# Kernel optimization log

Measured on AMD Instinct MI355X. Metric: run time of the kernel, lower is better.

Reference implementation:

```python
import jax, jax.numpy as jnp
import numpy as np

B, T, I, H, O = 128, 256, 64, 1024, 64


def setup_inputs() -> dict:
    key = jax.random.key(0)
    ks = jax.random.split(key, 16)
    s_ih1 = 1.0 / np.sqrt(H)
    def mk(k, shape, s):
        return jax.random.uniform(k, shape, jnp.float32, -s, s)
    return {
        "x": jax.random.normal(ks[0], (B, T, I), jnp.float32),
        # RNNCell 1: input I -> hidden H
        "W_ih1": mk(ks[1], (H, I), s_ih1),
        "b_ih1": mk(ks[2], (H,), s_ih1),
        "W_hh1": mk(ks[3], (H, H), s_ih1),
        "b_hh1": mk(ks[4], (H,), s_ih1),
        # RNNCell 2: hidden H -> hidden H
        "W_ih2": mk(ks[5], (H, H), s_ih1),
        "b_ih2": mk(ks[6], (H,), s_ih1),
        "W_hh2": mk(ks[7], (H, H), s_ih1),
        "b_hh2": mk(ks[8], (H,), s_ih1),
        # gate: 2H -> H
        "Wg": mk(ks[9], (H, 2 * H), 1.0 / np.sqrt(2 * H)),
        "bg": mk(ks[10], (H,), 1.0 / np.sqrt(2 * H)),
        # output heads: H -> O
        "Wo1": mk(ks[11], (O, H), s_ih1),
        "bo1": mk(ks[12], (O,), s_ih1),
        "Wo2": mk(ks[13], (O, H), s_ih1),
        "bo2": mk(ks[14], (O,), s_ih1),
    }


def reference(x, W_ih1, b_ih1, W_hh1, b_hh1, W_ih2, b_ih2, W_hh2, b_hh2,
              Wg, bg, Wo1, bo1, Wo2, bo2):
    batch = x.shape[0]
    h1_0 = jnp.zeros((batch, H), x.dtype)
    h2_0 = jnp.zeros((batch, H), x.dtype)
    u_0 = jnp.ones((batch, H), x.dtype)

    def step(carry, x_t):
        h1, h2, u = carry
        # RNNCell 1
        h1 = jnp.tanh(x_t @ W_ih1.T + b_ih1 + h1 @ W_hh1.T + b_hh1)
        # RNNCell 2, gated convex blend with previous h2
        h2_new = jnp.tanh(h1 @ W_ih2.T + b_ih2 + h2 @ W_hh2.T + b_hh2)
        h2 = u * h2_new + (1.0 - u) * h2
        # dual tanh output head
        out = jnp.tanh(h1 @ Wo1.T + bo1) + jnp.tanh(h2 @ Wo2.T + bo2)
        # gate for NEXT step, computed from current hiddens
        u = jax.nn.sigmoid(jnp.concatenate([h1, h2], axis=1) @ Wg.T + bg)
        return (h1, h2, u), out

    xs = jnp.swapaxes(x, 0, 1)  # [T, B, I]
    _, outs = jax.lax.scan(step, (h1_0, h2_0, u_0), xs)
    return jnp.swapaxes(outs, 0, 1)  # [B, T, O]
```

## Files before the change

kernel.cpp:

```cpp
#include <hip/hip_runtime.h>
#include <cstddef>

using bf16x8 = __attribute__((ext_vector_type(8))) short;
using f32x4  = __attribute__((ext_vector_type(4))) float;

constexpr int Bb = 128;
constexpr int Tt = 256;
constexpr int Hh = 1024;
constexpr int Oo = 64;
constexpr int NBLK = 168;
constexpr int FLAG_STRIDE = 32;
constexpr int RS = 1048;

__device__ __forceinline__ float bf2f(short s) {
  unsigned int u = ((unsigned int)(unsigned short)s) << 16;
  float f;
  __builtin_memcpy(&f, &u, 4);
  return f;
}
__device__ __forceinline__ short f2bf(float f) {
  unsigned int u;
  __builtin_memcpy(&u, &f, 4);
  u += 0x7fffu + ((u >> 16) & 1u);
  return (short)(u >> 16);
}
__device__ __forceinline__ bf16x8 as_bf(int4 v) {
  union { int4 i; bf16x8 b; } u; u.i = v; return u.b;
}
__device__ __forceinline__ float ldf(const float* p) {
  return __hip_atomic_load((float*)p, __ATOMIC_RELAXED, __HIP_MEMORY_SCOPE_AGENT);
}
__device__ __forceinline__ void stf(float* p, float v) {
  __hip_atomic_store(p, v, __ATOMIC_RELAXED, __HIP_MEMORY_SCOPE_AGENT);
}
__device__ __forceinline__ unsigned ldu(const unsigned* p) {
  return __hip_atomic_load((unsigned*)p, __ATOMIC_RELAXED, __HIP_MEMORY_SCOPE_AGENT);
}

#define LD16A(d, p) asm volatile("global_load_dwordx4 %0, %1, off sc1" \
                                 : "=v"(d) : "v"((const void*)(p)))

__device__ __forceinline__ void stage32(short* As, const short* src, int tid) {
  const int row = tid >> 3;
  const int c0  = (tid & 7) * 8;
  const short* gp = src + (size_t)row * Hh + c0;
  short* lp = As + row * RS + c0;
  int4 r0[8], r1[8];
#pragma unroll
  for (int j = 0; j < 8; ++j) LD16A(r0[j], gp + j * 64);
#pragma unroll
  for (int j = 0; j < 8; ++j) LD16A(r1[j], gp + 512 + j * 64);
  asm volatile("s_waitcnt vmcnt(8)" ::: "memory");
#pragma unroll
  for (int j = 0; j < 8; ++j) *(int4*)(lp + j * 64) = r0[j];
  asm volatile("s_waitcnt vmcnt(0)" ::: "memory");
#pragma unroll
  for (int j = 0; j < 8; ++j) *(int4*)(lp + 512 + j * 64) = r1[j];
}

struct BPre {
  const short *bp0, *bp1;
  int4 b0v[6], b1v[6];
};
__device__ __forceinline__ void prefillB(BPre& P,
    const short* __restrict__ B0, size_t st0,
    const short* __restrict__ B1, size_t st1, int lm, int q) {
  P.bp0 = B0 + (size_t)lm * st0 + q * 8;
  P.bp1 = B1 + (size_t)lm * st1 + q * 8;
#pragma unroll
  for (int c = 0; c < 5; ++c) {
    P.b0v[c] = *(const int4*)(P.bp0 + c * 32);
    P.b1v[c] = *(const int4*)(P.bp1 + c * 32);
  }
}
__device__ __forceinline__ void pass32p(const short* As, int lm, int q,
    BPre& P, f32x4 (&acc)[2][2]) {
  const short* ap0 = As + lm * RS + q * 8;
  const short* ap1 = ap0 + 16 * RS;
#pragma unroll
  for (int c = 0; c < 32; ++c) {
    if (c + 5 < 32) {
      P.b0v[(c + 5) % 6] = *(const int4*)(P.bp0 + (c + 5) * 32);
      P.b1v[(c + 5) % 6] = *(const int4*)(P.bp1 + (c + 5) * 32);
    }
    const bf16x8 a0 = as_bf(*(const int4*)(ap0 + c * 32));
    const bf16x8 a1 = as_bf(*(const int4*)(ap1 + c * 32));
    const bf16x8 b0 = as_bf(P.b0v[c % 6]);
    const bf16x8 b1 = as_bf(P.b1v[c % 6]);
    acc[0][0] = __builtin_amdgcn_mfma_f32_16x16x32_bf16(a0, b0, acc[0][0], 0, 0, 0);
    acc[0][1] = __builtin_amdgcn_mfma_f32_16x16x32_bf16(a1, b0, acc[0][1], 0, 0, 0);
    acc[1][0] = __builtin_amdgcn_mfma_f32_16x16x32_bf16(a0, b1, acc[1][0], 0, 0, 0);
    acc[1][1] = __builtin_amdgcn_mfma_f32_16x16x32_bf16(a1, b1, acc[1][1], 0, 0, 0);
  }
}

__device__ __forceinline__ void grid_barrier(unsigned* flags,
                                             unsigned gen, int bid, int tid) {
  __builtin_amdgcn_s_waitcnt(0);
  __syncthreads();
  if (tid == 0)
    __hip_atomic_store(flags + (size_t)bid * FLAG_STRIDE, gen,
                       __ATOMIC_RELAXED, __HIP_MEMORY_SCOPE_AGENT);
  if (tid < 64) {
    const unsigned* f = flags + (size_t)tid * FLAG_STRIDE;
    for (;;) {
      const unsigned a = ldu(f);
      const unsigned b = ldu(f +  64 * FLAG_STRIDE);
      const unsigned c = ldu(f + 128 * FLAG_STRIDE);
      if (__all((a >= gen) && (b >= gen) && (c >= gen))) break;
      __builtin_amdgcn_s_sleep(1);
    }
  }
  __syncthreads();
  asm volatile("" ::: "memory");
}

#define ST_BF16_PAIR(BASE, ROW, COL, HV) do {                              \
    const int _ov = __shfl_xor((int)(unsigned short)(HV), 1, 64);          \
    if ((lm & 1) == 0) {                                                   \
      const unsigned _pk = (unsigned)(unsigned short)(HV) | ((unsigned)_ov << 16); \
      __hip_atomic_store((unsigned*)((BASE) + (size_t)(ROW) * Hh + (COL)), _pk, \
                         __ATOMIC_RELAXED, __HIP_MEMORY_SCOPE_AGENT);      \
    } } while (0)

struct RP {
  short *h1a, *h1b;
  short *h2a, *h2b;
  float *h2f;
  float *pre2f;
  float *pg1f;
  float *po1f;
  const short* prex;
  const short *whh1, *wih2, *whh2, *wg, *wo1, *wo2;
  const float *b_ih2, *b_hh2, *bg, *bo1, *bo2;
  float* out;
  unsigned *flags;
};

__global__ void __launch_bounds__(256, 1) rnn_kernel(RP p) {
  __shared__ short As[32 * RS];
  const int tid = threadIdx.x;
  const int lane = tid & 63;
  const int wv = tid >> 6;
  const int lm = lane & 15;
  const int q = lane >> 4;
  const int bid = blockIdx.x;

  int role, mb, cb;
  if      (bid < 32)  { role = 0; mb = (bid >> 3) * 32;         cb = (bid & 7) * 128; }
  else if (bid < 64)  { role = 1; mb = ((bid - 32) >> 3) * 32;  cb = ((bid - 32) & 7) * 128; }
  else if (bid < 96)  { role = 2; mb = ((bid - 64) >> 3) * 32;  cb = ((bid - 64) & 7) * 128; }
  else if (bid < 100) { role = 3; mb = (bid - 96) * 32;         cb = 0; }
  else if (bid < 164) { role = 4; mb = ((bid - 100) >> 4) * 32; cb = ((bid - 100) & 15) * 64; }
  else                { role = 5; mb = (bid - 164) * 32;        cb = 0; }

  int colw;
  if (role == 4) colw = cb + wv * 16;
  else if (role == 3 || role == 5) colw = (wv & 1) * 32;
  else colw = cb + wv * 32;

  float bias0 = 0.f, bias1 = 0.f;
  if (role == 1) {
    bias0 = p.b_ih2[colw + lm] + p.b_hh2[colw + lm];
    bias1 = p.b_ih2[colw + 16 + lm] + p.b_hh2[colw + 16 + lm];
  } else if (role == 2) {
    bias0 = p.bg[colw + lm]; bias1 = p.bg[colw + 16 + lm];
  } else if (role == 3) {
    bias0 = p.bo1[colw + lm]; bias1 = p.bo1[colw + 16 + lm];
  } else if (role == 5) {
    bias0 = p.bo2[colw + lm]; bias1 = p.bo2[colw + 16 + lm];
  }

  const short* B0; const short* B1;
  size_t st0 = Hh, st1 = Hh;
  if      (role == 0) { B0 = p.whh1 + (size_t)colw * Hh; B1 = p.whh1 + (size_t)(colw + 16) * Hh; }
  else if (role == 1) { B0 = p.wih2 + (size_t)colw * Hh; B1 = p.wih2 + (size_t)(colw + 16) * Hh; }
  else if (role == 2) { B0 = p.wg + (size_t)colw * (2 * Hh); B1 = p.wg + (size_t)(colw + 16) * (2 * Hh); st0 = st1 = 2 * Hh; }
  else if (role == 3) { B0 = p.wo1 + (size_t)colw * Hh; B1 = p.wo1 + (size_t)(colw + 16) * Hh; }
  else if (role == 4) { B0 = p.whh2 + (size_t)colw * Hh; B1 = p.wg + Hh + (size_t)colw * (2 * Hh); st1 = 2 * Hh; }
  else                { B0 = p.wo2 + (size_t)colw * Hh; B1 = p.wo2 + (size_t)(colw + 16) * Hh; }

  const size_t HS = (size_t)Bb * Hh;
  const f32x4 z4 = {0.f, 0.f, 0.f, 0.f};
  unsigned gen = 0;

  for (int ph = 0; ph <= Tt + 2; ++ph) {
    const short* h1prev = (ph & 1) ? p.h1a : p.h1b;
    short*       h1out  = (ph & 1) ? p.h1b : p.h1a;
    const int s = ph - 2;
    const short* h2prev = (s & 1) ? p.h2a : p.h2b;
    short*       h2out  = (s & 1) ? p.h2b : p.h2a;

    if (role == 0) {
      if (ph < Tt) {
        BPre P; prefillB(P, B0, st0, B1, st1, lm, q);
        short prs[2][2][4];
        const short* pr = p.prex + (size_t)ph * HS;
#pragma unroll
        for (int n = 0; n < 2; ++n)
#pragma unroll
          for (int rf = 0; rf < 2; ++rf)
#pragma unroll
            for (int r = 0; r < 4; ++r)
              prs[n][rf][r] = pr[(size_t)(mb + rf * 16 + q * 4 + r) * Hh + colw + n * 16 + lm];
        stage32(As, h1prev + (size_t)mb * Hh, tid);
        __syncthreads();
        f32x4 acc[2][2]; acc[0][0] = acc[0][1] = acc[1][0] = acc[1][1] = z4;
        pass32p(As, lm, q, P, acc);
#pragma unroll
        for (int n = 0; n < 2; ++n)
#pragma unroll
          for (int rf = 0; rf < 2; ++rf)
#pragma unroll
            for (int r = 0; r < 4; ++r) {
              const int row = mb + rf * 16 + q * 4 + r;
              const int col = colw + n * 16 + lm;
              const short hv = f2bf(tanhf(acc[n][rf][r] + bf2f(prs[n][rf][r])));
              ST_BF16_PAIR(h1out, row, col, hv);
            }
      }
    } else if (role == 1) {
      if (ph >= 1 && ph <= Tt) {
        BPre P; prefillB(P, B0, st0, B1, st1, lm, q);
        float* dst = p.pre2f + (size_t)((ph - 1) & 1) * HS;
        stage32(As, h1prev + (size_t)mb * Hh, tid);
        __syncthreads();
        f32x4 acc[2][2]; acc[0][0] = acc[0][1] = acc[1][0] = acc[1][1] = z4;
        pass32p(As, lm, q, P, acc);
#pragma unroll
        for (int n = 0; n < 2; ++n)
#pragma unroll
          for (int rf = 0; rf < 2; ++rf)
#pragma unroll
            for (int r = 0; r < 4; ++r) {
              const int row = mb + rf * 16 + q * 4 + r;
              const int col = colw + n * 16 + lm;
              stf(dst + (size_t)row * Hh + col, acc[n][rf][r] + (n ? bias1 : bias0));
            }
      }
    } else if (role == 2) {
      if (ph >= 1 && ph <= Tt) {
        BPre P; prefillB(P, B0, st0, B1, st1, lm, q);
        float* dst = p.pg1f + (size_t)((ph - 1) % 3) * HS;
        stage32(As, h1prev + (size_t)mb * Hh, tid);
        __syncthreads();
        f32x4 acc[2][2]; acc[0][0] = acc[0][1] = acc[1][0] = acc[1][1] = z4;
        pass32p(As, lm, q, P, acc);
#pragma unroll
        for (int n = 0; n < 2; ++n)
#pragma unroll
          for (int rf = 0; rf < 2; ++rf)
#pragma unroll
            for (int r = 0; r < 4; ++r) {
              const int row = mb + rf * 16 + q * 4 + r;
              const int col = colw + n * 16 + lm;
              stf(dst + (size_t)row * Hh + col, acc[n][rf][r] + (n ? bias1 : bias0));
            }
      }
    } else if (role == 3) {
      if (ph >= 1 && ph <= Tt) {
        BPre P;
        if (wv < 2) prefillB(P, B0, st0, B1, st1, lm, q);
        float* dst = p.po1f + (size_t)((ph - 1) % 3) * (Bb * Oo);
        stage32(As, h1prev + (size_t)mb * Hh, tid);
        __syncthreads();
        if (wv < 2) {
          f32x4 acc[2][2]; acc[0][0] = acc[0][1] = acc[1][0] = acc[1][1] = z4;
          pass32p(As, lm, q, P, acc);
#pragma unroll
          for (int n = 0; n < 2; ++n)
#pragma unroll
            for (int rf = 0; rf < 2; ++rf)
#pragma unroll
              for (int r = 0; r < 4; ++r) {
                const int row = mb + rf * 16 + q * 4 + r;
                const int col = colw + n * 16 + lm;
                stf(dst + (size_t)row * Oo + col,
                    tanhf(acc[n][rf][r] + (n ? bias1 : bias0)));
              }
        }
      }
    } else if (role == 4) {
      if (ph >= 2 && ph <= Tt + 1) {
        BPre P; prefillB(P, B0, st0, B1, st1, lm, q);
        float p2v[2][4], pg1v[2][4], hpv[2][4];
        const float* pre2s = p.pre2f + (size_t)(s & 1) * HS;
        const float* pg1s  = p.pg1f + (size_t)((s + 2) % 3) * HS;
#pragma unroll
        for (int rf = 0; rf < 2; ++rf)
#pragma unroll
          for (int r = 0; r < 4; ++r) {
            const size_t idx = (size_t)(mb + rf * 16 + q * 4 + r) * Hh + colw + lm;
            p2v[rf][r] = ldf(pre2s + idx);
            pg1v[rf][r] = (s > 0) ? ldf(pg1s + idx) : 0.f;
            hpv[rf][r] = p.h2f[idx];
          }
        stage32(As, h2prev + (size_t)mb * Hh, tid);
        __syncthreads();
        f32x4 acc[2][2]; acc[0][0] = acc[0][1] = acc[1][0] = acc[1][1] = z4;
        pass32p(As, lm, q, P, acc);
#pragma unroll
        for (int rf = 0; rf < 2; ++rf)
#pragma unroll
          for (int r = 0; r < 4; ++r) {
            const int row = mb + rf * 16 + q * 4 + r;
            const int col = colw + lm;
            const size_t idx = (size_t)row * Hh + col;
            const float u = (s == 0) ? 1.f
                : 1.f / (1.f + expf(-(acc[1][rf][r] + pg1v[rf][r])));
            const float hn = tanhf(acc[0][rf][r] + p2v[rf][r]);
            const float nv = fmaf(u, hn - hpv[rf][r], hpv[rf][r]);
            p.h2f[idx] = nv;
            const short hv = f2bf(nv);
            ST_BF16_PAIR(h2out, row, col, hv);
          }
      }
    } else {
      if (ph >= 3) {
        const int to = ph - 3;
        BPre P;
        if (wv < 2) prefillB(P, B0, st0, B1, st1, lm, q);
        const float* po1s = p.po1f + (size_t)(to % 3) * (Bb * Oo);
        float pv[2][2][4];
        if (wv < 2) {
#pragma unroll
          for (int n = 0; n < 2; ++n)
#pragma unroll
            for (int rf = 0; rf < 2; ++rf)
#pragma unroll
              for (int r = 0; r < 4; ++r)
                pv[n][rf][r] = ldf(po1s + (size_t)(mb + rf * 16 + q * 4 + r) * Oo
                                   + colw + n * 16 + lm);
        }
        stage32(As, h2prev + (size_t)mb * Hh, tid);
        __syncthreads();
        if (wv < 2) {
          f32x4 acc[2][2]; acc[0][0] = acc[0][1] = acc[1][0] = acc[1][1] = z4;
          pass32p(As, lm, q, P, acc);
#pragma unroll
          for (int n = 0; n < 2; ++n)
#pragma unroll
            for (int rf = 0; rf < 2; ++rf)
#pragma unroll
              for (int r = 0; r < 4; ++r) {
                const int row = mb + rf * 16 + q * 4 + r;
                const int col = colw + n * 16 + lm;
                p.out[(size_t)row * (Tt * Oo) + (size_t)to * Oo + col] =
                    pv[n][rf][r] + tanhf(acc[n][rf][r] + (n ? bias1 : bias0));
              }
        }
      }
    }
    ++gen;
    grid_barrier(p.flags, gen, bid, tid);
  }
}

__global__ void __launch_bounds__(256) prex_kernel(
    const float* __restrict__ x, const float* __restrict__ wih1,
    const float* __restrict__ b_ih1, const float* __restrict__ b_hh1,
    short* __restrict__ prex) {
  const int tid = threadIdx.x;
  const int lane = tid & 63;
  const int wv = tid >> 6;
  const int lm = lane & 15;
  const int q = lane >> 4;
  const int bm = blockIdx.x >> 4;
  const int bn = blockIdx.x & 15;
  const int rowbase = bm * 64;
  const int col = bn * 64 + wv * 16 + lm;

  const f32x4 z4 = {0.f, 0.f, 0.f, 0.f};
  f32x4 acc[4];
#pragma unroll
  for (int mt = 0; mt < 4; ++mt) acc[mt] = z4;

#pragma unroll
  for (int kc = 0; kc < 2; ++kc) {
    const float* bp = wih1 + col * 64 + kc * 32 + q * 8;
    bf16x8 bf;
#pragma unroll
    for (int j = 0; j < 8; ++j) bf[j] = f2bf(bp[j]);
#pragma unroll
    for (int mt = 0; mt < 4; ++mt) {
      const float* ap = x + (size_t)(rowbase + mt * 16 + lm) * 64 + kc * 32 + q * 8;
      bf16x8 af;
#pragma unroll
      for (int j = 0; j < 8; ++j) af[j] = f2bf(ap[j]);
      acc[mt] = __builtin_amdgcn_mfma_f32_16x16x32_bf16(af, bf, acc[mt], 0, 0, 0);
    }
  }
  const float bia = b_ih1[col] + b_hh1[col];
#pragma unroll
  for (int mt = 0; mt < 4; ++mt) {
#pragma unroll
    for (int r = 0; r < 4; ++r) {
      const int row = rowbase + mt * 16 + q * 4 + r;
      const int b  = row >> 8;
      const int tt = row & 255;
      prex[((size_t)tt * Bb + b) * Hh + col] = f2bf(acc[mt][r] + bia);
    }
  }
}

__global__ void conv_kernel(const float* __restrict__ s, short* __restrict__ d, int n) {
  int i = blockIdx.x * blockDim.x + threadIdx.x;
  const int stride = gridDim.x * blockDim.x;
  for (; i < n; i += stride) d[i] = f2bf(s[i]);
}

__global__ void init_kernel(short* h1a, short* h1b, short* h2a, short* h2b,
                            float* h2f, unsigned* flags) {
  const int i = blockIdx.x * blockDim.x + threadIdx.x;
  h1a[i] = 0; h1b[i] = 0; h2a[i] = 0; h2b[i] = 0; h2f[i] = 0.f;
  if (i < 256) flags[i * FLAG_STRIDE] = (i < NBLK) ? 0u : 0xFFFFFFFFu;
}

extern "C" void kernel_launch(void* const* d_in, const int* in_sizes, int n_in,
                              void* d_out, int out_size, void* d_ws, size_t ws_size,
                              hipStream_t stream) {
  (void)in_sizes; (void)n_in; (void)out_size; (void)ws_size;
  const float* x      = (const float*)d_in[0];
  const float* W_ih1  = (const float*)d_in[1];
  const float* b_ih1  = (const float*)d_in[2];
  const float* W_hh1  = (const float*)d_in[3];
  const float* b_hh1  = (const float*)d_in[4];
  const float* W_ih2  = (const float*)d_in[5];
  const float* b_ih2  = (const float*)d_in[6];
  const float* W_hh2  = (const float*)d_in[7];
  const float* b_hh2  = (const float*)d_in[8];
  const float* Wg     = (const float*)d_in[9];
  const float* bg     = (const float*)d_in[10];
  const float* Wo1    = (const float*)d_in[11];
  const float* bo1    = (const float*)d_in[12];
  const float* Wo2    = (const float*)d_in[13];
  const float* bo2    = (const float*)d_in[14];

  char* ws = (char*)d_ws;
  size_t off = 0;
  auto alloc = [&](size_t bytes) -> void* {
    void* ptr = ws + off;
    off += (bytes + 255) & ~(size_t)255;
    return ptr;
  };
  short* whh1 = (short*)alloc((size_t)Hh * Hh * 2);
  short* wih2 = (short*)alloc((size_t)Hh * Hh * 2);
  short* whh2 = (short*)alloc((size_t)Hh * Hh * 2);
  short* wg   = (short*)alloc((size_t)Hh * 2 * Hh * 2);
  short* wo1  = (short*)alloc((size_t)Oo * Hh * 2);
  short* wo2  = (short*)alloc((size_t)Oo * Hh * 2);
  short* prex = (short*)alloc((size_t)Bb * Tt * Hh * 2);
  short* h1a  = (short*)alloc((size_t)Bb * Hh * 2);
  short* h1b  = (short*)alloc((size_t)Bb * Hh * 2);
  short* h2a  = (short*)alloc((size_t)Bb * Hh * 2);
  short* h2b  = (short*)alloc((size_t)Bb * Hh * 2);
  float* h2f  = (float*)alloc((size_t)Bb * Hh * 4);
  float* pre2f= (float*)alloc((size_t)2 * Bb * Hh * 4);
  float* pg1f = (float*)alloc((size_t)3 * Bb * Hh * 4);
  float* po1f = (float*)alloc((size_t)3 * Bb * Oo * 4);
  unsigned* flags = (unsigned*)alloc(256 * FLAG_STRIDE * 4);

  conv_kernel<<<1024, 256, 0, stream>>>(W_hh1, whh1, Hh * Hh);
  conv_kernel<<<1024, 256, 0, stream>>>(W_ih2, wih2, Hh * Hh);
  conv_kernel<<<1024, 256, 0, stream>>>(W_hh2, whh2, Hh * Hh);
  conv_kernel<<<2048, 256, 0, stream>>>(Wg,    wg,   Hh * 2 * Hh);
  conv_kernel<<<256,  256, 0, stream>>>(Wo1,   wo1,  Oo * Hh);
  conv_kernel<<<256,  256, 0, stream>>>(Wo2,   wo2,  Oo * Hh);
  init_kernel<<<512, 256, 0, stream>>>(h1a, h1b, h2a, h2b, h2f, flags);
  prex_kernel<<<8192, 256, 0, stream>>>(x, W_ih1, b_ih1, b_hh1, prex);

  RP p;
  p.h1a = h1a; p.h1b = h1b; p.h2a = h2a; p.h2b = h2b;
  p.h2f = h2f; p.pre2f = pre2f; p.pg1f = pg1f; p.po1f = po1f;
  p.prex = prex;
  p.whh1 = whh1; p.wih2 = wih2; p.whh2 = whh2;
  p.wg = wg; p.wo1 = wo1; p.wo2 = wo2;
  p.b_ih2 = b_ih2; p.b_hh2 = b_hh2;
  p.bg = bg; p.bo1 = bo1; p.bo2 = bo2;
  p.out = (float*)d_out;
  p.flags = flags;

  rnn_kernel<<<NBLK, 256, 0, stream>>>(p);
}
```

Measured before the change: 3.234 ms.

## Replace global grid barrier with per-role dataflow flags and triple-buffered state

Removes the all-block grid barrier after each phase and replaces it with per-producer generation flags, so each role polls only the producer groups it depends on. Hidden-state buffers become triple-buffered and the intermediate buffers get three or four slots, which lets roles run a few steps apart without overwriting data still being read. This aims to cut barrier latency and let the h1 chain run ahead of the h2 chain. The cost is more complex dependency tracking, where a wrong slot count or wait condition could cause races.

```diff
diff --git a/kernel.cpp b/kernel.cpp
--- a/kernel.cpp
+++ b/kernel.cpp
@@ -12,6 +12,13 @@
 constexpr int FLAG_STRIDE = 32;
 constexpr int RS = 1048;
 
+constexpr int FH1 = 0;
+constexpr int FP2 = 32;
+constexpr int FPG = 64;
+constexpr int FPO = 96;
+constexpr int FH2 = 100;
+constexpr int FZO = 164;
+
 __device__ __forceinline__ float bf2f(short s) {
   unsigned int u = ((unsigned int)(unsigned short)s) << 16;
   float f;
@@ -35,6 +42,13 @@
 }
 __device__ __forceinline__ unsigned ldu(const unsigned* p) {
   return __hip_atomic_load((unsigned*)p, __ATOMIC_RELAXED, __HIP_MEMORY_SCOPE_AGENT);
+}
+__device__ __forceinline__ short* sel3(short* a, short* b, short* c, int i) {
+  return i == 0 ? a : (i == 1 ? b : c);
+}
+__device__ __forceinline__ const short* sel3c(const short* a, const short* b,
+                                              const short* c, int i) {
+  return i == 0 ? a : (i == 1 ? b : c);
 }
 
 #define LD16A(d, p) asm volatile("global_load_dwordx4 %0, %1, off sc1" \
@@ -94,26 +108,20 @@
   }
 }
 
-__device__ __forceinline__ void grid_barrier(unsigned* flags,
-                                             unsigned gen, int bid, int tid) {
-  __builtin_amdgcn_s_waitcnt(0);
-  __syncthreads();
-  if (tid == 0)
-    __hip_atomic_store(flags + (size_t)bid * FLAG_STRIDE, gen,
-                       __ATOMIC_RELAXED, __HIP_MEMORY_SCOPE_AGENT);
-  if (tid < 64) {
-    const unsigned* f = flags + (size_t)tid * FLAG_STRIDE;
-    for (;;) {
-      const unsigned a = ldu(f);
-      const unsigned b = ldu(f +  64 * FLAG_STRIDE);
-      const unsigned c = ldu(f + 128 * FLAG_STRIDE);
-      if (__all((a >= gen) && (b >= gen) && (c >= gen))) break;
-      __builtin_amdgcn_s_sleep(1);
-    }
-  }
-  __syncthreads();
-  asm volatile("" ::: "memory");
-}
+__device__ __forceinline__ void poll_ge(const unsigned* flags, int base,
+                                        int mask, unsigned gen) {
+  const unsigned* f = flags + (size_t)(base + (threadIdx.x & mask)) * FLAG_STRIDE;
+  while (!__all(ldu(f) >= gen))
+    __builtin_amdgcn_s_sleep(2);
+}
+
+#define POST_FLAG(GEN) do {                                                \
+    asm volatile("s_waitcnt vmcnt(0) lgkmcnt(0)" ::: "memory");            \
+    __syncthreads();                                                       \
+    if (tid == 0)                                                          \
+      __hip_atomic_store(p.flags + (size_t)bid * FLAG_STRIDE, (unsigned)(GEN), \
+                         __ATOMIC_RELAXED, __HIP_MEMORY_SCOPE_AGENT);      \
+  } while (0)
 
 #define ST_BF16_PAIR(BASE, ROW, COL, HV) do {                              \
     const int _ov = __shfl_xor((int)(unsigned short)(HV), 1, 64);          \
@@ -124,8 +132,8 @@
     } } while (0)
 
 struct RP {
-  short *h1a, *h1b;
-  short *h2a, *h2b;
+  short *h1r0, *h1r1, *h1r2;
+  short *h2r0, *h2r1, *h2r2;
   float *h2f;
   float *pre2f;
   float *pg1f;
@@ -134,7 +142,7 @@
   const short *whh1, *wih2, *whh2, *wg, *wo1, *wo2;
   const float *b_ih2, *b_hh2, *bg, *bo1, *bo2;
   float* out;
-  unsigned *flags;
+  unsigned* flags;
 };
 
 __global__ void __launch_bounds__(256, 1) rnn_kernel(RP p) {
@@ -182,31 +190,115 @@
 
   const size_t HS = (size_t)Bb * Hh;
   const f32x4 z4 = {0.f, 0.f, 0.f, 0.f};
-  unsigned gen = 0;
-
-  for (int ph = 0; ph <= Tt + 2; ++ph) {
-    const short* h1prev = (ph & 1) ? p.h1a : p.h1b;
-    short*       h1out  = (ph & 1) ? p.h1b : p.h1a;
-    const int s = ph - 2;
-    const short* h2prev = (s & 1) ? p.h2a : p.h2b;
-    short*       h2out  = (s & 1) ? p.h2b : p.h2a;
-
-    if (role == 0) {
-      if (ph < Tt) {
-        BPre P; prefillB(P, B0, st0, B1, st1, lm, q);
-        short prs[2][2][4];
-        const short* pr = p.prex + (size_t)ph * HS;
-#pragma unroll
-        for (int n = 0; n < 2; ++n)
-#pragma unroll
-          for (int rf = 0; rf < 2; ++rf)
-#pragma unroll
-            for (int r = 0; r < 4; ++r)
-              prs[n][rf][r] = pr[(size_t)(mb + rf * 16 + q * 4 + r) * Hh + colw + n * 16 + lm];
-        stage32(As, h1prev + (size_t)mb * Hh, tid);
-        __syncthreads();
+
+  if (role == 0) {
+    for (int t = 0; t < Tt; ++t) {
+      BPre P; prefillB(P, B0, st0, B1, st1, lm, q);
+      short prs[2][2][4];
+      const short* pr = p.prex + (size_t)t * HS;
+#pragma unroll
+      for (int n = 0; n < 2; ++n)
+#pragma unroll
+        for (int rf = 0; rf < 2; ++rf)
+#pragma unroll
+          for (int r = 0; r < 4; ++r)
+            prs[n][rf][r] = pr[(size_t)(mb + rf * 16 + q * 4 + r) * Hh + colw + n * 16 + lm];
+      if (tid < 64) {
+        if (t >= 1) poll_ge(p.flags, FH1, 31, (unsigned)t);
+        if (t >= 3) {
+          poll_ge(p.flags, FP2, 31, (unsigned)(t - 2));
+          poll_ge(p.flags, FPG, 31, (unsigned)(t - 2));
+          poll_ge(p.flags, FPO, 3,  (unsigned)(t - 2));
+        }
+      }
+      __syncthreads();
+      const short* h1prev = sel3c(p.h1r0, p.h1r1, p.h1r2, (t + 2) % 3);
+      stage32(As, h1prev + (size_t)mb * Hh, tid);
+      __syncthreads();
+      f32x4 acc[2][2]; acc[0][0] = acc[0][1] = acc[1][0] = acc[1][1] = z4;
+      pass32p(As, lm, q, P, acc);
+      short* h1out = sel3(p.h1r0, p.h1r1, p.h1r2, t % 3);
+#pragma unroll
+      for (int n = 0; n < 2; ++n)
+#pragma unroll
+        for (int rf = 0; rf < 2; ++rf)
+#pragma unroll
+          for (int r = 0; r < 4; ++r) {
+            const int row = mb + rf * 16 + q * 4 + r;
+            const int col = colw + n * 16 + lm;
+            const short hv = f2bf(tanhf(acc[n][rf][r] + bf2f(prs[n][rf][r])));
+            ST_BF16_PAIR(h1out, row, col, hv);
+          }
+      POST_FLAG(t + 1);
+    }
+  } else if (role == 1) {
+    for (int t = 0; t < Tt; ++t) {
+      BPre P; prefillB(P, B0, st0, B1, st1, lm, q);
+      if (tid < 64) {
+        poll_ge(p.flags, FH1, 31, (unsigned)(t + 1));
+        if (t >= 3) poll_ge(p.flags, FH2, 63, (unsigned)(t - 2));
+      }
+      __syncthreads();
+      const short* h1cur = sel3c(p.h1r0, p.h1r1, p.h1r2, t % 3);
+      stage32(As, h1cur + (size_t)mb * Hh, tid);
+      __syncthreads();
+      f32x4 acc[2][2]; acc[0][0] = acc[0][1] = acc[1][0] = acc[1][1] = z4;
+      pass32p(As, lm, q, P, acc);
+      float* dst = p.pre2f + (size_t)(t % 3) * HS;
+#pragma unroll
+      for (int n = 0; n < 2; ++n)
+#pragma unroll
+        for (int rf = 0; rf < 2; ++rf)
+#pragma unroll
+          for (int r = 0; r < 4; ++r) {
+            const int row = mb + rf * 16 + q * 4 + r;
+            const int col = colw + n * 16 + lm;
+            stf(dst + (size_t)row * Hh + col, acc[n][rf][r] + (n ? bias1 : bias0));
+          }
+      POST_FLAG(t + 1);
+    }
+  } else if (role == 2) {
+    for (int t = 0; t < Tt; ++t) {
+      BPre P; prefillB(P, B0, st0, B1, st1, lm, q);
+      if (tid < 64) {
+        poll_ge(p.flags, FH1, 31, (unsigned)(t + 1));
+        if (t >= 4) poll_ge(p.flags, FH2, 63, (unsigned)(t - 2));
+      }
+      __syncthreads();
+      const short* h1cur = sel3c(p.h1r0, p.h1r1, p.h1r2, t % 3);
+      stage32(As, h1cur + (size_t)mb * Hh, tid);
+      __syncthreads();
+      f32x4 acc[2][2]; acc[0][0] = acc[0][1] = acc[1][0] = acc[1][1] = z4;
+      pass32p(As, lm, q, P, acc);
+      float* dst = p.pg1f + (size_t)(t % 4) * HS;
+#pragma unroll
+      for (int n = 0; n < 2; ++n)
+#pragma unroll
+        for (int rf = 0; rf < 2; ++rf)
+#pragma unroll
+          for (int r = 0; r < 4; ++r) {
+            const int row = mb + rf * 16 + q * 4 + r;
+            const int col = colw + n * 16 + lm;
+            stf(dst + (size_t)row * Hh + col, acc[n][rf][r] + (n ? bias1 : bias0));
+          }
+      POST_FLAG(t + 1);
+    }
+  } else if (role == 3) {
+    for (int t = 0; t < Tt; ++t) {
+      BPre P;
+      if (wv < 2) prefillB(P, B0, st0, B1, st1, lm, q);
+      if (tid < 64) {
+        poll_ge(p.flags, FH1, 31, (unsigned)(t + 1));
+        if (t >= 4) poll_ge(p.flags, FZO, 3, (unsigned)(t - 3));
+      }
+      __syncthreads();
+      const short* h1cur = sel3c(p.h1r0, p.h1r1, p.h1r2, t % 3);
+      stage32(As, h1cur + (size_t)mb * Hh, tid);
+      __syncthreads();
+      if (wv < 2) {
         f32x4 acc[2][2]; acc[0][0] = acc[0][1] = acc[1][0] = acc[1][1] = z4;
         pass32p(As, lm, q, P, acc);
+        float* dst = p.po1f + (size_t)(t % 4) * (Bb * Oo);
 #pragma unroll
         for (int n = 0; n < 2; ++n)
 #pragma unroll
@@ -215,16 +307,84 @@
             for (int r = 0; r < 4; ++r) {
               const int row = mb + rf * 16 + q * 4 + r;
               const int col = colw + n * 16 + lm;
-              const short hv = f2bf(tanhf(acc[n][rf][r] + bf2f(prs[n][rf][r])));
-              ST_BF16_PAIR(h1out, row, col, hv);
+              stf(dst + (size_t)row * Oo + col,
+                  tanhf(acc[n][rf][r] + (n ? bias1 : bias0)));
             }
       }
-    } else if (role == 1) {
-      if (ph >= 1 && ph <= Tt) {
-        BPre P; prefillB(P, B0, st0, B1, st1, lm, q);
-        float* dst = p.pre2f + (size_t)((ph - 1) & 1) * HS;
-        stage32(As, h1prev + (size_t)mb * Hh, tid);
-        __syncthreads();
+      POST_FLAG(t + 1);
+    }
+  } else if (role == 4) {
+    for (int s = 0; s < Tt; ++s) {
+      BPre P; prefillB(P, B0, st0, B1, st1, lm, q);
+      if (tid < 64) {
+        poll_ge(p.flags, FP2, 31, (unsigned)(s + 1));
+        if (s >= 1) {
+          poll_ge(p.flags, FPG, 31, (unsigned)s);
+          poll_ge(p.flags, FH2, 63, (unsigned)s);
+        }
+        if (s >= 3) poll_ge(p.flags, FZO, 3, (unsigned)(s - 2));
+      }
+      __syncthreads();
+      float p2v[2][4], pg1v[2][4], hpv[2][4];
+      const float* pre2s = p.pre2f + (size_t)(s % 3) * HS;
+      const float* pg1s  = p.pg1f + (size_t)((s + 3) % 4) * HS;
+#pragma unroll
+      for (int rf = 0; rf < 2; ++rf)
+#pragma unroll
+        for (int r = 0; r < 4; ++r) {
+          const size_t idx = (size_t)(mb + rf * 16 + q * 4 + r) * Hh + colw + lm;
+          p2v[rf][r] = ldf(pre2s + idx);
+          pg1v[rf][r] = (s > 0) ? ldf(pg1s + idx) : 0.f;
+          hpv[rf][r] = p.h2f[idx];
+        }
+      const short* h2prev = sel3c(p.h2r0, p.h2r1, p.h2r2, (s + 2) % 3);
+      stage32(As, h2prev + (size_t)mb * Hh, tid);
+      __syncthreads();
+      f32x4 acc[2][2]; acc[0][0] = acc[0][1] = acc[1][0] = acc[1][1] = z4;
+      pass32p(As, lm, q, P, acc);
+      short* h2out = sel3(p.h2r0, p.h2r1, p.h2r2, s % 3);
+#pragma unroll
+      for (int rf = 0; rf < 2; ++rf)
+#pragma unroll
+        for (int r = 0; r < 4; ++r) {
+          const int row = mb + rf * 16 + q * 4 + r;
+          const int col = colw + lm;
+          const size_t idx = (size_t)row * Hh + col;
+          const float u = (s == 0) ? 1.f
+              : 1.f / (1.f + expf(-(acc[1][rf][r] + pg1v[rf][r])));
+          const float hn = tanhf(acc[0][rf][r] + p2v[rf][r]);
+          const float nv = fmaf(u, hn - hpv[rf][r], hpv[rf][r]);
+          p.h2f[idx] = nv;
+          const short hv = f2bf(nv);
+          ST_BF16_PAIR(h2out, row, col, hv);
+        }
+      POST_FLAG(s + 1);
+    }
+  } else {
+    for (int ot = 0; ot < Tt; ++ot) {
+      BPre P;
+      if (wv < 2) prefillB(P, B0, st0, B1, st1, lm, q);
+      if (tid < 64) {
+        poll_ge(p.flags, FH2, 63, (unsigned)(ot + 1));
+        poll_ge(p.flags, FPO, 3,  (unsigned)(ot + 1));
+      }
+      __syncthreads();
+      const float* po1s = p.po1f + (size_t)(ot % 4) * (Bb * Oo);
+      float pv[2][2][4];
+      if (wv < 2) {
+#pragma unroll
+        for (int n = 0; n < 2; ++n)
+#pragma unroll
+          for (int rf = 0; rf < 2; ++rf)
+#pragma unroll
+            for (int r = 0; r < 4; ++r)
+              pv[n][rf][r] = ldf(po1s + (size_t)(mb + rf * 16 + q * 4 + r) * Oo
+                                 + colw + n * 16 + lm);
+      }
+      const short* h2cur = sel3c(p.h2r0, p.h2r1, p.h2r2, ot % 3);
+      stage32(As, h2cur + (size_t)mb * Hh, tid);
+      __syncthreads();
+      if (wv < 2) {
         f32x4 acc[2][2]; acc[0][0] = acc[0][1] = acc[1][0] = acc[1][1] = z4;
         pass32p(As, lm, q, P, acc);
 #pragma unroll
@@ -235,124 +395,12 @@
             for (int r = 0; r < 4; ++r) {
               const int row = mb + rf * 16 + q * 4 + r;
               const int col = colw + n * 16 + lm;
-              stf(dst + (size_t)row * Hh + col, acc[n][rf][r] + (n ? bias1 : bias0));
+              p.out[(size_t)row * (Tt * Oo) + (size_t)ot * Oo + col] =
+                  pv[n][rf][r] + tanhf(acc[n][rf][r] + (n ? bias1 : bias0));
             }
       }
-    } else if (role == 2) {
-      if (ph >= 1 && ph <= Tt) {
-        BPre P; prefillB(P, B0, st0, B1, st1, lm, q);
-        float* dst = p.pg1f + (size_t)((ph - 1) % 3) * HS;
-        stage32(As, h1prev + (size_t)mb * Hh, tid);
-        __syncthreads();
-        f32x4 acc[2][2]; acc[0][0] = acc[0][1] = acc[1][0] = acc[1][1] = z4;
-        pass32p(As, lm, q, P, acc);
-#pragma unroll
-        for (int n = 0; n < 2; ++n)
-#pragma unroll
-          for (int rf = 0; rf < 2; ++rf)
-#pragma unroll
-            for (int r = 0; r < 4; ++r) {
-              const int row = mb + rf * 16 + q * 4 + r;
-              const int col = colw + n * 16 + lm;
-              stf(dst + (size_t)row * Hh + col, acc[n][rf][r] + (n ? bias1 : bias0));
-            }
-      }
-    } else if (role == 3) {
-      if (ph >= 1 && ph <= Tt) {
-        BPre P;
-        if (wv < 2) prefillB(P, B0, st0, B1, st1, lm, q);
-        float* dst = p.po1f + (size_t)((ph - 1) % 3) * (Bb * Oo);
-        stage32(As, h1prev + (size_t)mb * Hh, tid);
-        __syncthreads();
-        if (wv < 2) {
-          f32x4 acc[2][2]; acc[0][0] = acc[0][1] = acc[1][0] = acc[1][1] = z4;
-          pass32p(As, lm, q, P, acc);
-#pragma unroll
-          for (int n = 0; n < 2; ++n)
-#pragma unroll
-            for (int rf = 0; rf < 2; ++rf)
-#pragma unroll
-              for (int r = 0; r < 4; ++r) {
-                const int row = mb + rf * 16 + q * 4 + r;
-                const int col = colw + n * 16 + lm;
-                stf(dst + (size_t)row * Oo + col,
-                    tanhf(acc[n][rf][r] + (n ? bias1 : bias0)));
-              }
-        }
-      }
-    } else if (role == 4) {
-      if (ph >= 2 && ph <= Tt + 1) {
-        BPre P; prefillB(P, B0, st0, B1, st1, lm, q);
-        float p2v[2][4], pg1v[2][4], hpv[2][4];
-        const float* pre2s = p.pre2f + (size_t)(s & 1) * HS;
-        const float* pg1s  = p.pg1f + (size_t)((s + 2) % 3) * HS;
-#pragma unroll
-        for (int rf = 0; rf < 2; ++rf)
-#pragma unroll
-          for (int r = 0; r < 4; ++r) {
-            const size_t idx = (size_t)(mb + rf * 16 + q * 4 + r) * Hh + colw + lm;
-            p2v[rf][r] = ldf(pre2s + idx);
-            pg1v[rf][r] = (s > 0) ? ldf(pg1s + idx) : 0.f;
-            hpv[rf][r] = p.h2f[idx];
-          }
-        stage32(As, h2prev + (size_t)mb * Hh, tid);
-        __syncthreads();
-        f32x4 acc[2][2]; acc[0][0] = acc[0][1] = acc[1][0] = acc[1][1] = z4;
-        pass32p(As, lm, q, P, acc);
-#pragma unroll
-        for (int rf = 0; rf < 2; ++rf)
-#pragma unroll
-          for (int r = 0; r < 4; ++r) {
-            const int row = mb + rf * 16 + q * 4 + r;
-            const int col = colw + lm;
-            const size_t idx = (size_t)row * Hh + col;
-            const float u = (s == 0) ? 1.f
-                : 1.f / (1.f + expf(-(acc[1][rf][r] + pg1v[rf][r])));
-            const float hn = tanhf(acc[0][rf][r] + p2v[rf][r]);
-            const float nv = fmaf(u, hn - hpv[rf][r], hpv[rf][r]);
-            p.h2f[idx] = nv;
-            const short hv = f2bf(nv);
-            ST_BF16_PAIR(h2out, row, col, hv);
-          }
-      }
-    } else {
-      if (ph >= 3) {
-        const int to = ph - 3;
-        BPre P;
-        if (wv < 2) prefillB(P, B0, st0, B1, st1, lm, q);
-        const float* po1s = p.po1f + (size_t)(to % 3) * (Bb * Oo);
-        float pv[2][2][4];
-        if (wv < 2) {
-#pragma unroll
-          for (int n = 0; n < 2; ++n)
-#pragma unroll
-            for (int rf = 0; rf < 2; ++rf)
-#pragma unroll
-              for (int r = 0; r < 4; ++r)
-                pv[n][rf][r] = ldf(po1s + (size_t)(mb + rf * 16 + q * 4 + r) * Oo
-                                   + colw + n * 16 + lm);
-        }
-        stage32(As, h2prev + (size_t)mb * Hh, tid);
-        __syncthreads();
-        if (wv < 2) {
-          f32x4 acc[2][2]; acc[0][0] = acc[0][1] = acc[1][0] = acc[1][1] = z4;
-          pass32p(As, lm, q, P, acc);
-#pragma unroll
-          for (int n = 0; n < 2; ++n)
-#pragma unroll
-            for (int rf = 0; rf < 2; ++rf)
-#pragma unroll
-              for (int r = 0; r < 4; ++r) {
-                const int row = mb + rf * 16 + q * 4 + r;
-                const int col = colw + n * 16 + lm;
-                p.out[(size_t)row * (Tt * Oo) + (size_t)to * Oo + col] =
-                    pv[n][rf][r] + tanhf(acc[n][rf][r] + (n ? bias1 : bias0));
-              }
-        }
-      }
-    }
-    ++gen;
-    grid_barrier(p.flags, gen, bid, tid);
+      POST_FLAG(ot + 1);
+    }
   }
 }
 
@@ -409,11 +457,14 @@
   for (; i < n; i += stride) d[i] = f2bf(s[i]);
 }
 
-__global__ void init_kernel(short* h1a, short* h1b, short* h2a, short* h2b,
+__global__ void init_kernel(short* h1r0, short* h1r1, short* h1r2,
+                            short* h2r0, short* h2r1, short* h2r2,
                             float* h2f, unsigned* flags) {
   const int i = blockIdx.x * blockDim.x + threadIdx.x;
-  h1a[i] = 0; h1b[i] = 0; h2a[i] = 0; h2b[i] = 0; h2f[i] = 0.f;
-  if (i < 256) flags[i * FLAG_STRIDE] = (i < NBLK) ? 0u : 0xFFFFFFFFu;
+  h1r0[i] = 0; h1r1[i] = 0; h1r2[i] = 0;
+  h2r0[i] = 0; h2r1[i] = 0; h2r2[i] = 0;
+  h2f[i] = 0.f;
+  if (i < 256) flags[i * FLAG_STRIDE] = 0u;
 }
 
 extern "C" void kernel_launch(void* const* d_in, const int* in_sizes, int n_in,
@@ -450,14 +501,16 @@
   short* wo1  = (short*)alloc((size_t)Oo * Hh * 2);
   short* wo2  = (short*)alloc((size_t)Oo * Hh * 2);
   short* prex = (short*)alloc((size_t)Bb * Tt * Hh * 2);
-  short* h1a  = (short*)alloc((size_t)Bb * Hh * 2);
-  short* h1b  = (short*)alloc((size_t)Bb * Hh * 2);
-  short* h2a  = (short*)alloc((size_t)Bb * Hh * 2);
-  short* h2b  = (short*)alloc((size_t)Bb * Hh * 2);
+  short* h1r0 = (short*)alloc((size_t)Bb * Hh * 2);
+  short* h1r1 = (short*)alloc((size_t)Bb * Hh * 2);
+  short* h1r2 = (short*)alloc((size_t)Bb * Hh * 2);
+  short* h2r0 = (short*)alloc((size_t)Bb * Hh * 2);
+  short* h2r1 = (short*)alloc((size_t)Bb * Hh * 2);
+  short* h2r2 = (short*)alloc((size_t)Bb * Hh * 2);
   float* h2f  = (float*)alloc((size_t)Bb * Hh * 4);
-  float* pre2f= (float*)alloc((size_t)2 * Bb * Hh * 4);
-  float* pg1f = (float*)alloc((size_t)3 * Bb * Hh * 4);
-  float* po1f = (float*)alloc((size_t)3 * Bb * Oo * 4);
+  float* pre2f= (float*)alloc((size_t)3 * Bb * Hh * 4);
+  float* pg1f = (float*)alloc((size_t)4 * Bb * Hh * 4);
+  float* po1f = (float*)alloc((size_t)4 * Bb * Oo * 4);
   unsigned* flags = (unsigned*)alloc(256 * FLAG_STRIDE * 4);
 
   conv_kernel<<<1024, 256, 0, stream>>>(W_hh1, whh1, Hh * Hh);
@@ -466,11 +519,12 @@
   conv_kernel<<<2048, 256, 0, stream>>>(Wg,    wg,   Hh * 2 * Hh);
   conv_kernel<<<256,  256, 0, stream>>>(Wo1,   wo1,  Oo * Hh);
   conv_kernel<<<256,  256, 0, stream>>>(Wo2,   wo2,  Oo * Hh);
-  init_kernel<<<512, 256, 0, stream>>>(h1a, h1b, h2a, h2b, h2f, flags);
+  init_kernel<<<512, 256, 0, stream>>>(h1r0, h1r1, h1r2, h2r0, h2r1, h2r2, h2f, flags);
   prex_kernel<<<8192, 256, 0, stream>>>(x, W_ih1, b_ih1, b_hh1, prex);
 
   RP p;
-  p.h1a = h1a; p.h1b = h1b; p.h2a = h2a; p.h2b = h2b;
+  p.h1r0 = h1r0; p.h1r1 = h1r1; p.h1r2 = h1r2;
+  p.h2r0 = h2r0; p.h2r1 = h2r1; p.h2r2 = h2r2;
   p.h2f = h2f; p.pre2f = pre2f; p.pg1f = pg1f; p.po1f = po1f;
   p.prex = prex;
   p.whh1 = whh1; p.wih2 = wih2; p.whh2 = whh2;
```

Measured after the change: 3.127 ms. -3.3%, faster.
